# Kernel optimization log

Measured on AMD Instinct MI355X. Metric: run time of the kernel, lower is better.

## Reference

```python
import jax, jax.numpy as jnp
import numpy as np

S, N, LAT, HID, NH, NLAYERS = 8, 128, 128, 384, 8, 6
HT, WT, DT = 128, 128, 128
DIN, DOUT, RAD, LEVELS, FED = 1169, 3 + 3 * 128, 3, 4, 64


def sincos1d(d, pos):
    # MAE-style 1d sincos embedding, d even -> [..., d]
    omega = 1.0 / (10000.0 ** (jnp.arange(d // 2, dtype=jnp.float32) / (d / 2.0)))
    ang = pos[..., None] * omega
    return jnp.concatenate([jnp.sin(ang), jnp.cos(ang)], axis=-1)


def flow_embed(f, Cd=FED):
    # get_3d_embedding(flows, 64, cat_coords=True) -> [..., 3*Cd+3] = 195
    div = jnp.arange(0, Cd, 2, dtype=jnp.float32) * (1000.0 / Cd)
    outs = []
    for a in range(3):
        ang = f[..., a, None] * div
        pe = jnp.stack([jnp.sin(ang), jnp.cos(ang)], axis=-1).reshape(f.shape[:-1] + (Cd,))
        outs.append(pe)
    return jnp.concatenate(outs + [f], axis=-1)


def avg_pool2(x):
    B, Sv, Cc, H, W = x.shape
    return x.reshape(B, Sv, Cc, H // 2, 2, W // 2, 2).mean(axis=(4, 6))


def pyramid(fm):
    pyr = [fm]
    for _ in range(LEVELS - 1):
        fm = avg_pool2(fm)
        pyr.append(fm)
    return pyr


def bilinear_sample(corr, xy):
    # corr: [B,S,N,H,W]; xy: [B,S,N,P,2] pixel coords (x indexes W, y indexes H); zero padding
    B, Sv, Nn, H, W = corr.shape
    cf = corr.reshape(B, Sv, Nn, H * W)
    x, y = xy[..., 0], xy[..., 1]
    x0f = jnp.floor(x); y0f = jnp.floor(y)
    wx, wy = x - x0f, y - y0f
    x0 = x0f.astype(jnp.int32); y0 = y0f.astype(jnp.int32)

    def gather(xi, yi):
        ok = ((xi >= 0) & (xi < W) & (yi >= 0) & (yi < H)).astype(cf.dtype)
        idx = jnp.clip(yi, 0, H - 1) * W + jnp.clip(xi, 0, W - 1)
        v = jnp.take_along_axis(cf, idx.reshape(B, Sv, Nn, -1), axis=-1).reshape(idx.shape)
        return v * ok

    v00 = gather(x0, y0); v01 = gather(x0 + 1, y0)
    v10 = gather(x0, y0 + 1); v11 = gather(x0 + 1, y0 + 1)
    return v00 * (1 - wx) * (1 - wy) + v01 * wx * (1 - wy) + v10 * (1 - wx) * wy + v11 * wx * wy


def corr_sample(pyr, targets, coords):
    # RAFT/CoTracker CorrBlock: per-level dense correlation then (2r+1)^2 window bilinear lookup
    d = jnp.arange(-RAD, RAD + 1, dtype=jnp.float32)
    delta = jnp.stack(jnp.meshgrid(d, d, indexing="ij"), axis=-1).reshape(-1, 2)  # [49,2]
    scale = 1.0 / jnp.sqrt(jnp.float32(targets.shape[-1]))
    outs = []
    for l, fm in enumerate(pyr):
        corr = jnp.einsum("bsnc,bschw->bsnhw", targets, fm) * scale
        xy = coords[..., None, :] / (2.0 ** l) + delta
        outs.append(bilinear_sample(corr, xy))
    return jnp.concatenate(outs, axis=-1)  # [B,S,N,196]


def layernorm(x, g, b):
    m = x.mean(-1, keepdims=True)
    v = x.var(-1, keepdims=True)
    return (x - m) / jnp.sqrt(v + 1e-5) * g + b


def attention(x, Wqkv, bq, Wo, bo):
    M, T, H = x.shape
    dh = H // NH
    qkv = (x @ Wqkv + bq).reshape(M, T, 3, NH, dh)
    q, k, v = qkv[:, :, 0], qkv[:, :, 1], qkv[:, :, 2]
    att = jax.nn.softmax(jnp.einsum("mthd,mshd->mhts", q, k) / jnp.sqrt(jnp.float32(dh)), axis=-1)
    o = jnp.einsum("mhts,mshd->mthd", att, v).reshape(M, T, H)
    return o @ Wo + bo


def updateformer(x, support, W_in, b_in, lnp, Wqkv, bqkv, Wo, bo, W1, b1, W2, b2, W_out, b_out, Ws, bs):
    # x: [B,N,T,DIN]; alternating time (over T) and space (over N) pre-LN transformer blocks
    B, Np, T, _ = x.shape
    sproj = support @ Ws + bs  # [100,HID]
    h = x @ W_in + b_in + sproj.mean(axis=0)
    for i in range(NLAYERS):
        g1, bb1, g2, bb2 = lnp[i, 0], lnp[i, 1], lnp[i, 2], lnp[i, 3]
        if i % 2 == 0:
            y = h.reshape(B * Np, T, HID)
        else:
            y = h.transpose(0, 2, 1, 3).reshape(B * T, Np, HID)
        y = y + attention(layernorm(y, g1, bb1), Wqkv[i], bqkv[i], Wo[i], bo[i])
        z = layernorm(y, g2, bb2)
        y = y + jax.nn.gelu(z @ W1[i] + b1[i], approximate=False) @ W2[i] + b2[i]
        if i % 2 == 0:
            h = y.reshape(B, Np, T, HID)
        else:
            h = y.reshape(B, T, Np, HID).transpose(0, 2, 1, 3)
    return h @ W_out + b_out, sproj[None]


def groupnorm1(x, g, b):
    m = x.mean(-1, keepdims=True)
    v = x.var(-1, keepdims=True)
    return (x - m) / jnp.sqrt(v + 1e-5) * g + b


def _forward(fmapXY, fmapYZ, fmapXZ, coords_init, vis_init, track_mask, feat_init, support_features,
             W_in, b_in, lnp, Wqkv, bqkv, Wo, bo, W1, b1, W2, b2, W_out, b_out, Ws, bs,
             gn_g, gn_b, Wu, bu, Wvis, bvis, iters):
    B, Sv, Cc, H, W = fmapXY.shape
    D = fmapXZ.shape[-2]
    Nn = coords_init.shape[2]
    coords = coords_init
    ffeats = [feat_init[..., k] for k in range(3)]
    pyrXY, pyrYZ, pyrXZ = pyramid(fmapXY), pyramid(fmapYZ), pyramid(fmapXZ)
    grid_size = jnp.array([H, W, D], dtype=jnp.float32)
    # 3d sincos pos embed from query coords; 1169 padded to 1170 -> 390/axis, truncated back
    g = (coords[:, 0] / grid_size * 2.0 - 1.0) * 128.0  # [B,N,3]
    pe = jnp.concatenate([sincos1d(390, g[..., i]) for i in range(3)], axis=-1)[..., :DIN]
    pos_embed = pe.reshape(B * Nn, 1, DIN)
    times_embed = sincos1d(1170, jnp.arange(Sv, dtype=jnp.float32))[None, :, :DIN]
    support = support_features
    for _ in range(iters):
        coords = jax.lax.stop_gradient(coords)  # matches coords.detach()
        fxy = corr_sample(pyrXY, ffeats[0], coords[..., :2])
        fyz = corr_sample(pyrYZ, ffeats[1], coords[..., 1:3])
        fxz = corr_sample(pyrXZ, ffeats[2], coords[..., 0::2])
        fcorrs = jnp.concatenate([fxy, fyz, fxz], axis=-1)  # [B,S,N,588]
        fcorrs_ = fcorrs.transpose(0, 2, 1, 3).reshape(B * Nn, Sv, -1)
        flows_ = (coords - coords[:, :1]).transpose(0, 2, 1, 3).reshape(B * Nn, Sv, 3)
        flows_cat = flow_embed(flows_)  # [BN,S,195]
        ff = [f.transpose(0, 2, 1, 3).reshape(B * Nn, Sv, LAT) for f in ffeats]
        ffeats_ = jnp.concatenate(ff, axis=-1)  # [BN,S,384]
        # replicate torch's cat(dim=2)+permute+reshape layout exactly
        tmv = jnp.concatenate([track_mask, vis_init], axis=2).transpose(0, 2, 1, 3).reshape(B * Nn, Sv, 2)
        tin = jnp.concatenate([flows_cat, fcorrs_, ffeats_, tmv], axis=-1)  # [BN,S,1169]
        x = (tin + pos_embed + times_embed).reshape(B, Nn, Sv, DIN)
        delta, dse3 = updateformer(x, support, W_in, b_in, lnp, Wqkv, bqkv, Wo, bo, W1, b1, W2, b2, W_out, b_out, Ws, bs)
        support = support + dse3[0] / 100.0
        delta = delta.reshape(B * Nn, Sv, DOUT)
        d_coord = delta[..., :3].reshape(B, Nn, Sv, 3).transpose(0, 2, 1, 3)
        coords = coords + d_coord
        new_ffeats = []
        for k in range(3):
            dfk = delta[..., 3 + k * LAT:3 + (k + 1) * LAT]
            upd = jax.nn.gelu(groupnorm1(dfk, gn_g[k], gn_b[k]) @ Wu[k] + bu[k], approximate=False)
            new_ffeats.append(ffeats[k] + upd.reshape(B, Nn, Sv, LAT).transpose(0, 2, 1, 3))
        ffeats = new_ffeats
    vis = (jnp.concatenate(ffeats, axis=-1) @ Wvis + bvis)[..., 0]  # [B,S,N]
    return jnp.concatenate([coords, vis[..., None]], axis=-1)  # [B,S,N,4]


def setup_inputs() -> dict:
    key = jax.random.key(0)
    ks = jax.random.split(key, 16)
    f32 = jnp.float32
    B = 1
    fmapXY = jax.random.normal(ks[0], (B, S, LAT, HT, WT), f32)
    fmapYZ = jax.random.normal(ks[1], (B, S, LAT, DT, HT), f32)
    fmapXZ = jax.random.normal(ks[2], (B, S, LAT, DT, WT), f32)
    coords_init = jax.random.uniform(ks[3], (B, S, N, 3), f32) * 112.0 + 8.0
    vis_init = jnp.ones((B, S, N, 1), f32)
    track_mask = jnp.ones((B, S, N, 1), f32)
    feat_init = jax.random.normal(ks[4], (B, S, N, LAT, 3), f32)
    support_features = jnp.zeros((100, HID), f32) + 0.1
    w = lambda k, sh: jax.random.normal(k, sh, f32) * 0.02
    ln1 = jnp.stack([jnp.ones(HID, f32), jnp.zeros(HID, f32), jnp.ones(HID, f32), jnp.zeros(HID, f32)])
    params = dict(
        W_in=w(ks[5], (DIN, HID)), b_in=jnp.zeros((HID,), f32),
        lnp=jnp.tile(ln1[None], (NLAYERS, 1, 1)),
        Wqkv=w(ks[6], (NLAYERS, HID, 3 * HID)), bqkv=jnp.zeros((NLAYERS, 3 * HID), f32),
        Wo=w(ks[7], (NLAYERS, HID, HID)), bo=jnp.zeros((NLAYERS, HID), f32),
        W1=w(ks[8], (NLAYERS, HID, 4 * HID)), b1=jnp.zeros((NLAYERS, 4 * HID), f32),
        W2=w(ks[9], (NLAYERS, 4 * HID, HID)), b2=jnp.zeros((NLAYERS, HID), f32),
        W_out=w(ks[10], (HID, DOUT)), b_out=jnp.zeros((DOUT,), f32),
        Ws=w(ks[11], (HID, HID)), bs=jnp.zeros((HID,), f32),
        gn_g=jnp.ones((3, LAT), f32), gn_b=jnp.zeros((3, LAT), f32),
        Wu=w(ks[12], (3, LAT, LAT)), bu=jnp.zeros((3, LAT), f32),
        Wvis=w(ks[13], (3 * LAT, 1)), bvis=jnp.zeros((1,), f32),
    )
    return dict(fmapXY=fmapXY, fmapYZ=fmapYZ, fmapXZ=fmapXZ, coords_init=coords_init,
                vis_init=vis_init, track_mask=track_mask, feat_init=feat_init,
                support_features=support_features, iters=2, **params)


def reference(fmapXY, fmapYZ, fmapXZ, coords_init, vis_init, track_mask, feat_init, support_features,
              W_in, b_in, lnp, Wqkv, bqkv, Wo, bo, W1, b1, W2, b2, W_out, b_out, Ws, bs,
              gn_g, gn_b, Wu, bu, Wvis, bvis, iters):
    return _forward(fmapXY, fmapYZ, fmapXZ, coords_init, vis_init, track_mask, feat_init, support_features,
                    W_in, b_in, lnp, Wqkv, bqkv, Wo, bo, W1, b1, W2, b2, W_out, b_out, Ws, bs,
                    gn_g, gn_b, Wu, bu, Wvis, bvis, iters)
```

## Files before the change

### kernel.cpp

```cpp
#include <hip/hip_runtime.h>
#include <hip/hip_bf16.h>


#define DEVFN __device__ __forceinline__

typedef __attribute__((ext_vector_type(8))) short short8;
typedef __attribute__((ext_vector_type(4))) float f32x4;

static constexpr float INV_SQRT_DH = 0.14433756729740643f;
static constexpr float CORR_SCALE  = 0.08838834764831845f;
static constexpr size_t VSTRIDE = 22282240;

DEVFN float gelu_exact(float x){
  return 0.5f * x * (1.0f + erff(x * 0.7071067811865476f));
}
DEVFN short bf16_of(float f){
  __hip_bfloat16 b = __float2bfloat16(f);
  return *reinterpret_cast<short*>(&b);
}
DEVFN float bfu(uint32_t u16){ return __uint_as_float(u16 << 16); }


__global__ void init_state_k(float* coords, const float* cinit,
                             float* ff, const float* feat_init,
                             float* support, const float* sfeat){
  int idx = blockIdx.x*256 + threadIdx.x;
  if (idx < 3072)  coords[idx]  = cinit[idx];
  if (idx < 49152){
    int row = idx / 384;
    support[idx] = (row < 100) ? sfeat[idx] : 0.0f;
  }
  if (idx < 393216){
    int k = idx / 131072, rest = idx % 131072;
    ff[idx] = feat_init[(size_t)rest*3 + k];
  }
}

__global__ void build_posE_k(float* posE, const float* cinit){
  int idx = blockIdx.x*256 + threadIdx.x;
  if (idx >= 128*1169) return;
  int n = idx / 1169, d = idx % 1169;
  int i = d / 390, dd = d % 390;
  float c = cinit[n*3 + i];
  float g = (c / 128.0f * 2.0f - 1.0f) * 128.0f;
  int m = (dd < 195) ? dd : dd - 195;
  float om = powf(10000.0f, -(float)m / 195.0f);
  float ang = g * om;
  posE[idx] = (dd < 195) ? sinf(ang) : cosf(ang);
}

__global__ void build_timE_k(float* timE){
  int idx = blockIdx.x*256 + threadIdx.x;
  if (idx >= 8*1169) return;
  int s = idx / 1169, d = idx % 1169;
  int m = (d < 585) ? d : d - 585;
  float om = powf(10000.0f, -(float)m / 585.0f);
  float ang = (float)s * om;
  timE[idx] = (d < 585) ? sinf(ang) : cosf(ang);
}

__global__ void transpose_cl_k(const float* __restrict__ in, __hip_bfloat16* __restrict__ out){
  __shared__ float tile[32][33];
  int s = blockIdx.z;
  int c0 = blockIdx.y*32, h0 = blockIdx.x*32;
  int tx = threadIdx.x & 31, ty = threadIdx.x >> 5;
  const float* ib = in + (size_t)s*128*16384;
  #pragma unroll
  for (int r=0;r<4;r++){
    int c = c0 + ty + r*8;
    tile[ty + r*8][tx] = ib[(size_t)c*16384 + h0 + tx];
  }
  __syncthreads();
  __hip_bfloat16* ob = out + (size_t)s*16384*128;
  #pragma unroll
  for (int r=0;r<4;r++){
    int hw = h0 + ty + r*8;
    ob[(size_t)hw*128 + c0 + tx] = __float2bfloat16(tile[tx][ty + r*8]);
  }
}

__global__ void pool2_k(const __hip_bfloat16* __restrict__ in, __hip_bfloat16* __restrict__ out, int So){
  int idx = blockIdx.x*256 + threadIdx.x;
  int total = 8*So*So*128;
  if (idx >= total) return;
  int c = idx & 127;
  int x = (idx >> 7) % So;
  int y = ((idx >> 7) / So) % So;
  int s = idx / (So*So*128);
  int Si = So*2;
  const __hip_bfloat16* b0 = in + (((size_t)s*Si + 2*y)*Si + 2*x)*128 + c;
  float v = __bfloat162float(b0[0]) + __bfloat162float(b0[128])
          + __bfloat162float(b0[(size_t)Si*128]) + __bfloat162float(b0[(size_t)Si*128 + 128]);
  out[idx] = __float2bfloat16(v*0.25f);
}

__global__ void wtrans_k(const float* __restrict__ in, __hip_bfloat16* __restrict__ out,
                         int K, int N, int Kpad, int Npad){
  __shared__ float tile[32][33];
  int z = blockIdx.z;
  const float* ib = in + (size_t)z*K*N;
  __hip_bfloat16* ob = out + (size_t)z*Npad*Kpad;
  int kb = blockIdx.y*32, nb = blockIdx.x*32;
  int tx = threadIdx.x & 31, ty = threadIdx.x >> 5;
  #pragma unroll
  for (int r=0;r<4;r++){
    int k = kb + ty + r*8, n = nb + tx;
    tile[ty+r*8][tx] = (k < K && n < N) ? ib[(size_t)k*N + n] : 0.0f;
  }
  __syncthreads();
  #pragma unroll
  for (int r=0;r<4;r++){
    int n = nb + ty + r*8, k = kb + tx;
    if (n < Npad && k < Kpad) ob[(size_t)n*Kpad + k] = __float2bfloat16(tile[tx][ty+r*8]);
  }
}

__global__ void assemble_x_k(__hip_bfloat16* __restrict__ xbuf, const float* __restrict__ posE,
                             const float* __restrict__ timE, const float* __restrict__ coords,
                             const float* __restrict__ ff, const float* __restrict__ tmask,
                             const float* __restrict__ vinit){
  int r = blockIdx.x;
  int n = r >> 3, s = r & 7;
  for (int d = threadIdx.x; d < 1184; d += blockDim.x){
    __hip_bfloat16* dst = xbuf + (size_t)r*1184 + d;
    if (d >= 1169){ *dst = __float2bfloat16(0.0f); continue; }
    float base = posE[(size_t)n*1169 + d] + timE[(size_t)s*1169 + d];
    if (d >= 195 && d < 783){ *dst = __float2bfloat16(base); continue; }
    float val;
    if (d < 195){
      if (d >= 192){
        int a = d - 192;
        val = coords[(s*128+n)*3 + a] - coords[n*3 + a];
      } else {
        int a = d >> 6, dd = d & 63;
        float f = coords[(s*128+n)*3 + a] - coords[n*3 + a];
        float ang = f * (31.25f * (float)(dd >> 1));
        val = (dd & 1) ? cosf(ang) : sinf(ang);
      }
    } else if (d < 1167){
      int cidx = d - 783, k = cidx >> 7, cc = cidx & 127;
      val = ff[(size_t)k*131072 + (size_t)(s*128+n)*128 + cc];
    } else {
      int c = d - 1167;
      int flat = n*16 + s*2 + c;
      int n2 = flat >> 3, s2 = flat & 7;
      val = (n2 < 128) ? tmask[s2*128 + n2] : vinit[s2*128 + (n2-128)];
    }
    *dst = __float2bfloat16(val + base);
  }
}

__global__ void corr_k(const __hip_bfloat16* __restrict__ pyr, const float* __restrict__ coords,
                       const float* __restrict__ ff, __hip_bfloat16* __restrict__ xbuf){
  __shared__ float t[128];
  __shared__ float p[64];
  int bid = blockIdx.x;
  int view = bid >> 10, s = (bid >> 7) & 7, n = bid & 127;
  int tid = threadIdx.x;
  t[tid]      = ff[(size_t)view*131072 + (size_t)(s*128+n)*128 + tid];
  t[tid + 64] = ff[(size_t)view*131072 + (size_t)(s*128+n)*128 + tid + 64];
  int ax = (view==1) ? 1 : 0;
  int ay = (view==0) ? 1 : 2;
  float X = coords[(s*128+n)*3 + ax];
  float Y = coords[(s*128+n)*3 + ay];
  const __hip_bfloat16* vb = pyr + (size_t)view*VSTRIDE;
  __syncthreads();
  size_t loff = 0;
  for (int l=0;l<4;l++){
    int sz = 128 >> l;
    float inv = 1.0f / (float)(1 << l);
    float cx = X * inv, cy = Y * inv;
    float x0f = floorf(cx), y0f = floorf(cy);
    float wx = cx - x0f, wy = cy - y0f;
    int ix0 = (int)x0f, iy0 = (int)y0f;
    int px = ix0 - 3 + (tid & 7);
    int py = iy0 - 3 + (tid >> 3);
    float acc = 0.0f;
    if (px >= 0 && px < sz && py >= 0 && py < sz){
      const uint2* row = reinterpret_cast<const uint2*>(vb + loff + (((size_t)s*sz + py)*sz + px)*128);
      #pragma unroll
      for (int c4=0;c4<32;c4++){
        uint2 u = row[c4];
        float f0 = __uint_as_float(u.x << 16);
        float f1 = __uint_as_float(u.x & 0xffff0000u);
        float f2 = __uint_as_float(u.y << 16);
        float f3 = __uint_as_float(u.y & 0xffff0000u);
        acc += t[c4*4+0]*f0 + t[c4*4+1]*f1 + t[c4*4+2]*f2 + t[c4*4+3]*f3;
      }
    }
    p[tid] = acc;
    __syncthreads();
    if (tid < 49){
      int i = tid / 7, jj = tid % 7;
      float v = p[jj*8+i]       * (1.0f-wx)*(1.0f-wy)
              + p[jj*8+i+1]     * wx*(1.0f-wy)
              + p[(jj+1)*8+i]   * (1.0f-wx)*wy
              + p[(jj+1)*8+i+1] * wx*wy;
      __hip_bfloat16* dst = xbuf + (size_t)(n*8+s)*1184 + 195 + view*196 + l*49 + tid;
      *dst = __float2bfloat16(__bfloat162float(*dst) + v * CORR_SCALE);
    }
    loff += (size_t)8*sz*sz*128;
    __syncthreads();
  }
}

__global__ void gn_rows_k(const float* __restrict__ dbuf,
                          const float* __restrict__ gn_g, const float* __restrict__ gn_b,
                          __hip_bfloat16* __restrict__ gtmp, float* __restrict__ coords){
  int k = blockIdx.y;
  const float* in = dbuf + 3 + k*128;
  const float* g = gn_g + k*128;
  const float* b = gn_b + k*128;
  __hip_bfloat16* out = gtmp + (size_t)k*131072;
  int wave = threadIdx.x >> 6, lane = threadIdx.x & 63;
  int r = blockIdx.x*4 + wave;
  const float* row = in + (size_t)r*387;
  float x0 = row[lane], x1 = row[lane+64];
  float sum = x0 + x1;
  #pragma unroll
  for (int o=32;o>0;o>>=1) sum += __shfl_xor(sum, o);
  float mean = sum / 128.0f;
  float d0 = x0-mean, d1 = x1-mean;
  float vs = d0*d0 + d1*d1;
  #pragma unroll
  for (int o=32;o>0;o>>=1) vs += __shfl_xor(vs, o);
  float invstd = 1.0f / sqrtf(vs/128.0f + 1e-5f);
  out[(size_t)r*128 + lane]      = __float2bfloat16(d0*invstd*g[lane] + b[lane]);
  out[(size_t)r*128 + lane + 64] = __float2bfloat16(d1*invstd*g[lane+64] + b[lane+64]);
  if (k == 0 && blockIdx.x < 12){
    int idx = blockIdx.x*256 + threadIdx.x;
    if (idx < 3072){
      int a = idx % 3, sn = idx / 3;
      int ss = sn >> 7, nn = sn & 127;
      coords[idx] += dbuf[(size_t)(nn*8+ss)*387 + a];
    }
  }
}

template<int K, int MODE, bool AF32>
__global__ __launch_bounds__(256) void mgemm_k(const void* __restrict__ A, int lda,
                                               const __hip_bfloat16* __restrict__ Bt,
                                               float* __restrict__ C, int ldc,
                                               int M, int N,
                                               const float* __restrict__ bias){
  constexpr int NSTEP = K/32;
  int tid = threadIdx.x;
  int lane = tid & 63, wid = tid >> 6;
  int wr = wid >> 1, wc = wid & 1;
  int lr = lane & 15, lk = lane >> 4;
  int m0 = blockIdx.y*64 + wr*32;
  int n0 = blockIdx.x*64 + wc*32;

  const __hip_bfloat16* Ab = (const __hip_bfloat16*)A;
  const float* Af = (const float*)A;
  size_t arow0 = (size_t)(m0 + lr)      * lda;
  size_t arow1 = (size_t)(m0 + 16 + lr) * lda;
  size_t brow0 = (size_t)(n0 + lr)      * K;
  size_t brow1 = (size_t)(n0 + 16 + lr) * K;

  f32x4 acc00 = {}, acc01 = {}, acc10 = {}, acc11 = {};

  auto loadAf = [&](size_t rowoff, int k0)->short8{
    if constexpr (AF32){
      const float* p = Af + rowoff + k0 + lk*8;
      short8 r;
      #pragma unroll
      for (int j=0;j<8;j++) r[j] = bf16_of(p[j]);
      return r;
    } else {
      return *reinterpret_cast<const short8*>(Ab + rowoff + k0 + lk*8);
    }
  };
  auto loadBf = [&](size_t rowoff, int k0)->short8{
    return *reinterpret_cast<const short8*>(Bt + rowoff + k0 + lk*8);
  };

  short8 a0 = loadAf(arow0,0), a1 = loadAf(arow1,0);
  short8 b0 = loadBf(brow0,0), b1 = loadBf(brow1,0);
  #pragma unroll
  for (int t=0;t<NSTEP;t++){
    short8 na0={}, na1={}, nb0={}, nb1={};
    if (t+1 < NSTEP){
      int k0 = (t+1)*32;
      na0 = loadAf(arow0,k0); na1 = loadAf(arow1,k0);
      nb0 = loadBf(brow0,k0); nb1 = loadBf(brow1,k0);
    }
    acc00 = __builtin_amdgcn_mfma_f32_16x16x32_bf16(a0,b0,acc00,0,0,0);
    acc01 = __builtin_amdgcn_mfma_f32_16x16x32_bf16(a0,b1,acc01,0,0,0);
    acc10 = __builtin_amdgcn_mfma_f32_16x16x32_bf16(a1,b0,acc10,0,0,0);
    acc11 = __builtin_amdgcn_mfma_f32_16x16x32_bf16(a1,b1,acc11,0,0,0);
    a0=na0; a1=na1; b0=nb0; b1=nb1;
  }

  f32x4 accs[2][2] = {{acc00, acc01},{acc10, acc11}};
  #pragma unroll
  for (int mi=0;mi<2;mi++){
    #pragma unroll
    for (int ni=0;ni<2;ni++){
      int c = n0 + ni*16 + lr;
      if (c >= N) continue;
      float bv = bias ? bias[c] : 0.0f;
      #pragma unroll
      for (int reg=0;reg<4;reg++){
        int r = m0 + mi*16 + lk*4 + reg;
        if (r >= M) continue;
        float v = accs[mi][ni][reg] + bv;
        if (MODE==0) C[(size_t)r*ldc + c] = v;
        else C[(size_t)r*ldc + c] += v;
      }
    }
  }
}

template<bool GELU>
__global__ __launch_bounds__(256) void lngemm_k(const float* __restrict__ A,
                                                const float* __restrict__ gamma,
                                                const float* __restrict__ beta,
                                                const __hip_bfloat16* __restrict__ Bt,
                                                __hip_bfloat16* __restrict__ Cbf, int ldc, int N,
                                                const float* __restrict__ bias){
  constexpr int LDSS = 392;
  __shared__ short Asm[64*LDSS];
  int tid = threadIdx.x, lane = tid & 63, w = tid >> 6;
  int m0 = blockIdx.y*64, n0b = blockIdx.x*64;

  float gg[6], bb[6];
  #pragma unroll
  for (int e=0;e<6;e++){ gg[e] = gamma[lane+e*64]; bb[e] = beta[lane+e*64]; }
  for (int rr=0; rr<16; rr++){
    int r = w*16 + rr;
    const float* row = A + (size_t)(m0+r)*384;
    float x[6]; float sum = 0.0f;
    #pragma unroll
    for (int e=0;e<6;e++){ x[e] = row[lane+e*64]; sum += x[e]; }
    #pragma unroll
    for (int o=32;o>0;o>>=1) sum += __shfl_xor(sum, o);
    float mean = sum * (1.0f/384.0f);
    float vs = 0.0f;
    #pragma unroll
    for (int e=0;e<6;e++){ float d = x[e]-mean; vs += d*d; }
    #pragma unroll
    for (int o=32;o>0;o>>=1) vs += __shfl_xor(vs, o);
    float invstd = 1.0f / sqrtf(vs*(1.0f/384.0f) + 1e-5f);
    #pragma unroll
    for (int e=0;e<6;e++)
      Asm[r*LDSS + lane + e*64] = bf16_of((x[e]-mean)*invstd*gg[e] + bb[e]);
  }
  __syncthreads();

  int wr = w >> 1, wc = w & 1;
  int lr = lane & 15, lk = lane >> 4;
  const __hip_bfloat16* Brow0 = Bt + (size_t)(n0b + wc*32 + lr)*384;
  const __hip_bfloat16* Brow1 = Brow0 + 16*384;
  short8 b0 = *(const short8*)(Brow0 + lk*8);
  short8 b1 = *(const short8*)(Brow1 + lk*8);
  f32x4 acc00={}, acc01={}, acc10={}, acc11={};
  #pragma unroll
  for (int t=0;t<12;t++){
    short8 a0 = *(const short8*)(&Asm[(wr*32+lr)*LDSS    + t*32 + lk*8]);
    short8 a1 = *(const short8*)(&Asm[(wr*32+16+lr)*LDSS + t*32 + lk*8]);
    short8 nb0={}, nb1={};
    if (t < 11){
      nb0 = *(const short8*)(Brow0 + (t+1)*32 + lk*8);
      nb1 = *(const short8*)(Brow1 + (t+1)*32 + lk*8);
    }
    acc00 = __builtin_amdgcn_mfma_f32_16x16x32_bf16(a0,b0,acc00,0,0,0);
    acc01 = __builtin_amdgcn_mfma_f32_16x16x32_bf16(a0,b1,acc01,0,0,0);
    acc10 = __builtin_amdgcn_mfma_f32_16x16x32_bf16(a1,b0,acc10,0,0,0);
    acc11 = __builtin_amdgcn_mfma_f32_16x16x32_bf16(a1,b1,acc11,0,0,0);
    b0=nb0; b1=nb1;
  }
  f32x4 accs[2][2] = {{acc00, acc01},{acc10, acc11}};
  #pragma unroll
  for (int mi=0;mi<2;mi++){
    #pragma unroll
    for (int ni=0;ni<2;ni++){
      int c = n0b + wc*32 + ni*16 + lr;
      float bv = bias[c];
      #pragma unroll
      for (int reg=0;reg<4;reg++){
        int r = m0 + wr*32 + mi*16 + lk*4 + reg;
        float v = accs[mi][ni][reg] + bv;
        Cbf[(size_t)r*ldc + c] = __float2bfloat16(GELU ? gelu_exact(v) : v);
      }
    }
  }
}

__global__ __launch_bounds__(256) void wu_gemm_k(const __hip_bfloat16* __restrict__ gtmp,
                                                 const __hip_bfloat16* __restrict__ WuT,
                                                 const float* __restrict__ bu,
                                                 float* __restrict__ ff){
  int z = blockIdx.z;
  const __hip_bfloat16* A  = gtmp + (size_t)z*131072;
  const __hip_bfloat16* Bt = WuT  + (size_t)z*16384;
  const float* bias = bu + (size_t)z*128;
  float* aux = ff + (size_t)z*131072;
  int tid = threadIdx.x, lane = tid & 63, wid = tid >> 6;
  int wr = wid >> 1, wc = wid & 1;
  int lr = lane & 15, lk = lane >> 4;
  int m0 = blockIdx.y*64 + wr*32;
  int n0 = blockIdx.x*64 + wc*32;
  const short8* A0 = (const short8*)(A + (size_t)(m0+lr)*128);
  const short8* A1 = (const short8*)(A + (size_t)(m0+16+lr)*128);
  const short8* B0 = (const short8*)(Bt + (size_t)(n0+lr)*128);
  const short8* B1 = (const short8*)(Bt + (size_t)(n0+16+lr)*128);
  f32x4 acc00={}, acc01={}, acc10={}, acc11={};
  #pragma unroll
  for (int t=0;t<4;t++){
    short8 a0 = A0[t*4 + lk], a1 = A1[t*4 + lk];
    short8 b0 = B0[t*4 + lk], b1 = B1[t*4 + lk];
    acc00 = __builtin_amdgcn_mfma_f32_16x16x32_bf16(a0,b0,acc00,0,0,0);
    acc01 = __builtin_amdgcn_mfma_f32_16x16x32_bf16(a0,b1,acc01,0,0,0);
    acc10 = __builtin_amdgcn_mfma_f32_16x16x32_bf16(a1,b0,acc10,0,0,0);
    acc11 = __builtin_amdgcn_mfma_f32_16x16x32_bf16(a1,b1,acc11,0,0,0);
  }
  f32x4 accs[2][2] = {{acc00, acc01},{acc10, acc11}};
  #pragma unroll
  for (int mi=0;mi<2;mi++){
    #pragma unroll
    for (int ni=0;ni<2;ni++){
      int c = n0 + ni*16 + lr;
      float bv = bias[c];
      #pragma unroll
      for (int reg=0;reg<4;reg++){
        int r = m0 + mi*16 + lk*4 + reg;
        float v = accs[mi][ni][reg] + bv;
        int ss = r & 7, nn2 = r >> 3;
        aux[((size_t)(ss*128+nn2))*128 + c] += gelu_exact(v);
      }
    }
  }
}

__global__ __launch_bounds__(512) void attn_even_k(const __hip_bfloat16* __restrict__ qkv,
                                                   __hip_bfloat16* __restrict__ attout){
  int g = blockIdx.x;
  int h = threadIdx.x >> 6;
  int lane = threadIdx.x & 63;
  int t = lane >> 3, j = lane & 7;
  const short* qs = (const short*)qkv;

  float q[48], kk[48];
  {
    const short8* qp = (const short8*)(qs + (size_t)(g*8+t)*1152 + h*48);
    const short8* kp = (const short8*)(qs + (size_t)(g*8+j)*1152 + 384 + h*48);
    #pragma unroll
    for (int c=0;c<6;c++){
      short8 qv = qp[c], kv = kp[c];
      #pragma unroll
      for (int e=0;e<8;e++){
        q[c*8+e]  = bfu((uint16_t)qv[e]);
        kk[c*8+e] = bfu((uint16_t)kv[e]);
      }
    }
  }
  float s = 0.0f;
  #pragma unroll
  for (int d=0;d<48;d++) s += q[d]*kk[d];
  s *= INV_SQRT_DH;
  float mx = s;
  #pragma unroll
  for (int o=1;o<8;o<<=1) mx = fmaxf(mx, __shfl_xor(mx, o));
  float e = expf(s - mx);
  float l = e;
  #pragma unroll
  for (int o=1;o<8;o<<=1) l += __shfl_xor(l, o);
  float p = e / l;

  float o6[6] = {0,0,0,0,0,0};
  #pragma unroll
  for (int jp=0;jp<8;jp++){
    float pj = __shfl(p, (lane & 56) | jp);
    const uint32_t* vp = (const uint32_t*)(qs + (size_t)(g*8+jp)*1152 + 768 + h*48 + j*6);
    uint32_t w0 = vp[0], w1 = vp[1], w2 = vp[2];
    o6[0] += pj * bfu(w0 & 0xffffu); o6[1] += pj * bfu(w0 >> 16);
    o6[2] += pj * bfu(w1 & 0xffffu); o6[3] += pj * bfu(w1 >> 16);
    o6[4] += pj * bfu(w2 & 0xffffu); o6[5] += pj * bfu(w2 >> 16);
  }
  uint32_t r0 = ((uint32_t)(uint16_t)bf16_of(o6[1]) << 16) | (uint16_t)bf16_of(o6[0]);
  uint32_t r1 = ((uint32_t)(uint16_t)bf16_of(o6[3]) << 16) | (uint16_t)bf16_of(o6[2]);
  uint32_t r2 = ((uint32_t)(uint16_t)bf16_of(o6[5]) << 16) | (uint16_t)bf16_of(o6[4]);
  uint32_t* op = (uint32_t*)((short*)attout + (size_t)(g*8+t)*384 + h*48 + j*6);
  op[0] = r0; op[1] = r1; op[2] = r2;
}

__global__ __launch_bounds__(256) void attn_odd_mfma_k(const __hip_bfloat16* __restrict__ qkv,
                                                       __hip_bfloat16* __restrict__ attout){
  __shared__ char smem[47872];
  short* Qb = (short*)smem;
  short* Kb = (short*)(smem + 18432);
  short* Pb = (short*)smem;
  short* Vt = (short*)(smem + 34816);
  int g = blockIdx.x & 7, h = blockIdx.x >> 3;
  int tid = threadIdx.x;

  const short* qs = (const short*)qkv;
  for (int idx = tid; idx < 768; idx += 256){
    int t = idx / 6, dblk = idx % 6;
    size_t base = (size_t)(t*8+g)*1152 + h*48 + dblk*8;
    *(short8*)(Qb + t*72 + dblk*8) = *(const short8*)(qs + base);
    *(short8*)(Kb + t*72 + dblk*8) = *(const short8*)(qs + base + 384);
  }
  short8 zz = {};
  for (int idx = tid; idx < 384; idx += 256){
    int t = idx / 3, dblk = idx % 3;
    *(short8*)(Qb + t*72 + 48 + dblk*8) = zz;
    *(short8*)(Kb + t*72 + 48 + dblk*8) = zz;
  }
  __syncthreads();

  int lane = tid & 63, w = tid >> 6;
  int lr = lane & 15, lk = lane >> 4;
  int m0 = w*32;

  f32x4 S[2][8] = {};
  #pragma unroll
  for (int ks=0; ks<2; ks++){
    short8 a0 = *(const short8*)(Qb + (m0+lr)*72    + ks*32 + lk*8);
    short8 a1 = *(const short8*)(Qb + (m0+16+lr)*72 + ks*32 + lk*8);
    #pragma unroll
    for (int ni=0; ni<8; ni++){
      short8 b = *(const short8*)(Kb + (ni*16+lr)*72 + ks*32 + lk*8);
      S[0][ni] = __builtin_amdgcn_mfma_f32_16x16x32_bf16(a0,b,S[0][ni],0,0,0);
      S[1][ni] = __builtin_amdgcn_mfma_f32_16x16x32_bf16(a1,b,S[1][ni],0,0,0);
    }
  }

  #pragma unroll
  for (int mi=0;mi<2;mi++){
    #pragma unroll
    for (int reg=0;reg<4;reg++){
      float m = -1e30f;
      #pragma unroll
      for (int ni=0;ni<8;ni++) m = fmaxf(m, S[mi][ni][reg]);
      #pragma unroll
      for (int o=1;o<16;o<<=1) m = fmaxf(m, __shfl_xor(m, o));
      m *= INV_SQRT_DH;
      float l = 0.0f;
      #pragma unroll
      for (int ni=0;ni<8;ni++){
        float p = expf(S[mi][ni][reg]*INV_SQRT_DH - m);
        S[mi][ni][reg] = p;
        l += p;
      }
      #pragma unroll
      for (int o=1;o<16;o<<=1) l += __shfl_xor(l, o);
      float inv = 1.0f/l;
      #pragma unroll
      for (int ni=0;ni<8;ni++) S[mi][ni][reg] *= inv;
    }
  }
  __syncthreads();

  for (int idx = tid; idx < 768; idx += 256){
    int j = idx / 6, dblk = idx % 6;
    short8 v = *(const short8*)(qs + (size_t)(j*8+g)*1152 + 768 + h*48 + dblk*8);
    #pragma unroll
    for (int e=0;e<8;e++) Vt[(dblk*8+e)*136 + j] = v[e];
  }
  #pragma unroll
  for (int mi=0;mi<2;mi++)
    #pragma unroll
    for (int ni=0;ni<8;ni++)
      #pragma unroll
      for (int reg=0;reg<4;reg++)
        Pb[(m0+mi*16+lk*4+reg)*136 + ni*16+lr] = bf16_of(S[mi][ni][reg]);
  __syncthreads();

  f32x4 O[2][3] = {};
  #pragma unroll
  for (int ks=0; ks<4; ks++){
    short8 a0 = *(const short8*)(Pb + (m0+lr)*136    + ks*32 + lk*8);
    short8 a1 = *(const short8*)(Pb + (m0+16+lr)*136 + ks*32 + lk*8);
    #pragma unroll
    for (int ni=0; ni<3; ni++){
      short8 b = *(const short8*)(Vt + (ni*16+lr)*136 + ks*32 + lk*8);
      O[0][ni] = __builtin_amdgcn_mfma_f32_16x16x32_bf16(a0,b,O[0][ni],0,0,0);
      O[1][ni] = __builtin_amdgcn_mfma_f32_16x16x32_bf16(a1,b,O[1][ni],0,0,0);
    }
  }
  #pragma unroll
  for (int mi=0;mi<2;mi++){
    #pragma unroll
    for (int ni=0;ni<3;ni++){
      #pragma unroll
      for (int reg=0;reg<4;reg++){
        int q = m0 + mi*16 + lk*4 + reg;
        int d = ni*16 + lr;
        attout[(size_t)(q*8+g)*384 + h*48 + d] = __float2bfloat16(O[mi][ni][reg]);
      }
    }
  }
}

__global__ void supp_smean_k(const float* __restrict__ sproj, const float* __restrict__ b_in,
                             float* __restrict__ bias2, float* __restrict__ support){
  int idx = blockIdx.x*256 + threadIdx.x;
  if (idx < 38400) support[idx] += sproj[idx]*0.01f;
  else if (idx < 38784){
    int c = idx - 38400;
    float s = 0.0f;
    for (int r=0;r<100;r++) s += sproj[r*384 + c];
    bias2[c] = b_in[c] + s*0.01f;
  }
}

__global__ void final_out_k(const float* __restrict__ coords, const float* __restrict__ ff,
                            const float* __restrict__ Wvis, const float* __restrict__ bvis,
                            float* __restrict__ out){
  int sn = blockIdx.x*64 + threadIdx.x;
  if (sn >= 1024) return;
  float acc = bvis[0];
  for (int k=0;k<3;k++)
    for (int c=0;c<128;c++)
      acc += ff[(size_t)k*131072 + (size_t)sn*128 + c] * Wvis[k*128 + c];
  out[sn*4+0] = coords[sn*3+0];
  out[sn*4+1] = coords[sn*3+1];
  out[sn*4+2] = coords[sn*3+2];
  out[sn*4+3] = acc;
}


extern "C" void kernel_launch(void* const* d_in, const int* in_sizes, int n_in,
                              void* d_out, int out_size, void* d_ws, size_t ws_size,
                              hipStream_t stream) {
  const float* fmapXY   = (const float*)d_in[0];
  const float* fmapYZ   = (const float*)d_in[1];
  const float* fmapXZ   = (const float*)d_in[2];
  const float* cinit    = (const float*)d_in[3];
  const float* vinit    = (const float*)d_in[4];
  const float* tmask    = (const float*)d_in[5];
  const float* feat_init= (const float*)d_in[6];
  const float* sfeat    = (const float*)d_in[7];
  const float* W_in     = (const float*)d_in[9];
  const float* b_in     = (const float*)d_in[10];
  const float* lnp      = (const float*)d_in[11];
  const float* Wqkv     = (const float*)d_in[12];
  const float* bqkv     = (const float*)d_in[13];
  const float* Wo       = (const float*)d_in[14];
  const float* bo       = (const float*)d_in[15];
  const float* W1       = (const float*)d_in[16];
  const float* b1       = (const float*)d_in[17];
  const float* W2       = (const float*)d_in[18];
  const float* b2       = (const float*)d_in[19];
  const float* W_out    = (const float*)d_in[20];
  const float* b_out    = (const float*)d_in[21];
  const float* Ws       = (const float*)d_in[22];
  const float* bs       = (const float*)d_in[23];
  const float* gn_g     = (const float*)d_in[24];
  const float* gn_b     = (const float*)d_in[25];
  const float* Wu       = (const float*)d_in[26];
  const float* bu       = (const float*)d_in[27];
  const float* Wvis     = (const float*)d_in[28];
  const float* bvis     = (const float*)d_in[29];
  const int ITERS = 2;

  char* wp = (char*)d_ws;
  auto alloc = [&](size_t bytes)->char* {
    char* p = wp; wp += (bytes + 255) & ~(size_t)255; return p;
  };
  __hip_bfloat16* pyr = (__hip_bfloat16*)alloc(3ull*VSTRIDE*2);
  float* coords = (float*)alloc(3072ull*4);
  float* ff     = (float*)alloc(393216ull*4);
  float* support= (float*)alloc(49152ull*4);
  float* sproj  = (float*)alloc(38400ull*4);
  float* bias2  = (float*)alloc(384ull*4);
  float* posE   = (float*)alloc(149632ull*4);
  float* timE   = (float*)alloc(9352ull*4);
  float* h      = (float*)alloc(393216ull*4);
  float* dbuf   = (float*)alloc(396288ull*4);
  __hip_bfloat16* xbuf_bf = (__hip_bfloat16*)alloc(1212416ull*2);
  __hip_bfloat16* qkv_bf  = (__hip_bfloat16*)alloc(1179648ull*2);
  __hip_bfloat16* atto_bf = (__hip_bfloat16*)alloc(393216ull*2);
  __hip_bfloat16* ffb_bf  = (__hip_bfloat16*)alloc(1572864ull*2);
  __hip_bfloat16* gtmp_bf = (__hip_bfloat16*)alloc(393216ull*2);
  __hip_bfloat16* WsT   = (__hip_bfloat16*)alloc(147456ull*2);
  __hip_bfloat16* WinT  = (__hip_bfloat16*)alloc(454656ull*2);
  __hip_bfloat16* WqkvT = (__hip_bfloat16*)alloc(2654208ull*2);
  __hip_bfloat16* WoT   = (__hip_bfloat16*)alloc(884736ull*2);
  __hip_bfloat16* W1T   = (__hip_bfloat16*)alloc(3538944ull*2);
  __hip_bfloat16* W2T   = (__hip_bfloat16*)alloc(3538944ull*2);
  __hip_bfloat16* WoutT = (__hip_bfloat16*)alloc(172032ull*2);
  __hip_bfloat16* WuT   = (__hip_bfloat16*)alloc(49152ull*2);
  if ((size_t)(wp - (char*)d_ws) > ws_size) return;

  init_state_k<<<1536, 256, 0, stream>>>(coords, cinit, ff, feat_init, support, sfeat);
  build_posE_k<<<(128*1169 + 255)/256, 256, 0, stream>>>(posE, cinit);
  build_timE_k<<<(8*1169 + 255)/256, 256, 0, stream>>>(timE);

  const float* fmaps[3] = {fmapXY, fmapYZ, fmapXZ};
  for (int v=0; v<3; v++){
    __hip_bfloat16* base = pyr + (size_t)v*VSTRIDE;
    transpose_cl_k<<<dim3(512,4,8), 256, 0, stream>>>(fmaps[v], base);
    pool2_k<<<(8*64*64*128 + 255)/256, 256, 0, stream>>>(base,              base + 16777216, 64);
    pool2_k<<<(8*32*32*128 + 255)/256, 256, 0, stream>>>(base + 16777216,   base + 20971520, 32);
    pool2_k<<<(8*16*16*128 + 255)/256, 256, 0, stream>>>(base + 20971520,   base + 22020096, 16);
  }

  wtrans_k<<<dim3(12,12,1), 256, 0, stream>>>(Ws,    WsT,   384, 384, 384, 384);
  wtrans_k<<<dim3(12,37,1), 256, 0, stream>>>(W_in,  WinT,  1169,384, 1184,384);
  wtrans_k<<<dim3(36,12,6), 256, 0, stream>>>(Wqkv,  WqkvT, 384, 1152,384, 1152);
  wtrans_k<<<dim3(12,12,6), 256, 0, stream>>>(Wo,    WoT,   384, 384, 384, 384);
  wtrans_k<<<dim3(48,12,6), 256, 0, stream>>>(W1,    W1T,   384, 1536,384, 1536);
  wtrans_k<<<dim3(12,48,6), 256, 0, stream>>>(W2,    W2T,   1536,384, 1536,384);
  wtrans_k<<<dim3(14,12,1), 256, 0, stream>>>(W_out, WoutT, 384, 387, 384, 448);
  wtrans_k<<<dim3(4,4,3),   256, 0, stream>>>(Wu,    WuT,   128, 128, 128, 128);

  for (int it=0; it<ITERS; ++it){
    assemble_x_k<<<1024, 256, 0, stream>>>(xbuf_bf, posE, timE, coords, ff, tmask, vinit);
    corr_k<<<3072, 64, 0, stream>>>(pyr, coords, ff, xbuf_bf);

    mgemm_k<384,0,true><<<dim3(6,2), 256, 0, stream>>>(support,384, WsT, sproj,384, 100,384, bs);
    supp_smean_k<<<152, 256, 0, stream>>>(sproj, b_in, bias2, support);

    mgemm_k<1184,0,false><<<dim3(6,16), 256, 0, stream>>>(xbuf_bf,1184, WinT, h,384, 1024,384, bias2);

    for (int i=0;i<6;i++){
      const float* g1  = lnp + (size_t)(i*4+0)*384;
      const float* bb1 = lnp + (size_t)(i*4+1)*384;
      const float* g2  = lnp + (size_t)(i*4+2)*384;
      const float* bb2 = lnp + (size_t)(i*4+3)*384;

      lngemm_k<false><<<dim3(18,16), 256, 0, stream>>>(h, g1, bb1, WqkvT + (size_t)i*442368,
                                                       qkv_bf, 1152, 1152, bqkv + i*1152);
      if ((i & 1) == 0) attn_even_k<<<128, 512, 0, stream>>>(qkv_bf, atto_bf);
      else              attn_odd_mfma_k<<<64, 256, 0, stream>>>(qkv_bf, atto_bf);
      mgemm_k<384,1,false><<<dim3(6,16), 256, 0, stream>>>(atto_bf,384, WoT + (size_t)i*147456,
                                                           h,384, 1024,384, bo + i*384);
      lngemm_k<true><<<dim3(24,16), 256, 0, stream>>>(h, g2, bb2, W1T + (size_t)i*589824,
                                                      ffb_bf, 1536, 1536, b1 + i*1536);
      mgemm_k<1536,1,false><<<dim3(6,16), 256, 0, stream>>>(ffb_bf,1536, W2T + (size_t)i*589824,
                                                            h,384, 1024,384, b2 + i*384);
    }

    mgemm_k<384,0,true><<<dim3(7,16), 256, 0, stream>>>(h,384, WoutT, dbuf,387, 1024,387, b_out);
    gn_rows_k<<<dim3(256,3), 256, 0, stream>>>(dbuf, gn_g, gn_b, gtmp_bf, coords);
    wu_gemm_k<<<dim3(2,16,3), 256, 0, stream>>>(gtmp_bf, WuT, bu, ff);
  }

  final_out_k<<<16, 64, 0, stream>>>(coords, ff, Wvis, bvis, (float*)d_out);
}
```

Before: 1.451 ms.

## Batch pyramid build across views, deepen GEMM prefetch, widen LN-GEMM tiles

Merges the per-view transpose and pooling launches into single launches that index the view through blockIdx.z, cutting launch count. The mgemm kernel now prefetches three K-steps ahead instead of one, to hide global load latency. lngemm widens each block to 128 output columns, each wave computing 4 N fragments with double-buffered B loads. The block count halves, so the LayerNorm prologue runs half as often, but fewer blocks run at once and register pressure rises.

```diff
diff --git a/kernel.cpp b/kernel.cpp
--- a/kernel.cpp
+++ b/kernel.cpp
@@ -59,9 +59,11 @@
   timE[idx] = (d < 585) ? sinf(ang) : cosf(ang);
 }
 
-__global__ void transpose_cl_k(const float* __restrict__ in, __hip_bfloat16* __restrict__ out){
+__global__ void transpose_cl_k(const float* __restrict__ inXY, const float* __restrict__ inYZ,
+                               const float* __restrict__ inXZ, __hip_bfloat16* __restrict__ pyr){
   __shared__ float tile[32][33];
-  int s = blockIdx.z;
+  int v = blockIdx.z >> 3, s = blockIdx.z & 7;
+  const float* in = (v==0) ? inXY : ((v==1) ? inYZ : inXZ);
   int c0 = blockIdx.y*32, h0 = blockIdx.x*32;
   int tx = threadIdx.x & 31, ty = threadIdx.x >> 5;
   const float* ib = in + (size_t)s*128*16384;
@@ -71,7 +73,7 @@
     tile[ty + r*8][tx] = ib[(size_t)c*16384 + h0 + tx];
   }
   __syncthreads();
-  __hip_bfloat16* ob = out + (size_t)s*16384*128;
+  __hip_bfloat16* ob = pyr + (size_t)v*VSTRIDE + (size_t)s*16384*128;
   #pragma unroll
   for (int r=0;r<4;r++){
     int hw = h0 + ty + r*8;
@@ -79,10 +81,12 @@
   }
 }
 
-__global__ void pool2_k(const __hip_bfloat16* __restrict__ in, __hip_bfloat16* __restrict__ out, int So){
+__global__ void pool2_k(__hip_bfloat16* __restrict__ pyr, size_t in_off, size_t out_off, int So){
   int idx = blockIdx.x*256 + threadIdx.x;
   int total = 8*So*So*128;
   if (idx >= total) return;
+  const __hip_bfloat16* in = pyr + (size_t)blockIdx.z*VSTRIDE + in_off;
+  __hip_bfloat16* out      = pyr + (size_t)blockIdx.z*VSTRIDE + out_off;
   int c = idx & 127;
   int x = (idx >> 7) % So;
   int y = ((idx >> 7) / So) % So;
@@ -258,38 +262,42 @@
   size_t brow0 = (size_t)(n0 + lr)      * K;
   size_t brow1 = (size_t)(n0 + 16 + lr) * K;
 
-  f32x4 acc00 = {}, acc01 = {}, acc10 = {}, acc11 = {};
-
-  auto loadAf = [&](size_t rowoff, int k0)->short8{
+  auto loadA = [&](size_t ro, int k0)->short8{
     if constexpr (AF32){
-      const float* p = Af + rowoff + k0 + lk*8;
+      const float* p = Af + ro + k0 + lk*8;
       short8 r;
       #pragma unroll
       for (int j=0;j<8;j++) r[j] = bf16_of(p[j]);
       return r;
     } else {
-      return *reinterpret_cast<const short8*>(Ab + rowoff + k0 + lk*8);
+      return *reinterpret_cast<const short8*>(Ab + ro + k0 + lk*8);
     }
   };
-  auto loadBf = [&](size_t rowoff, int k0)->short8{
-    return *reinterpret_cast<const short8*>(Bt + rowoff + k0 + lk*8);
+  auto loadB = [&](size_t ro, int k0)->short8{
+    return *reinterpret_cast<const short8*>(Bt + ro + k0 + lk*8);
   };
 
-  short8 a0 = loadAf(arow0,0), a1 = loadAf(arow1,0);
-  short8 b0 = loadBf(brow0,0), b1 = loadBf(brow1,0);
+  short8 a0[3], a1[3], b0[3], b1[3];
+  #pragma unroll
+  for (int p=0;p<3;p++){
+    if (p < NSTEP){
+      a0[p]=loadA(arow0,p*32); a1[p]=loadA(arow1,p*32);
+      b0[p]=loadB(brow0,p*32); b1[p]=loadB(brow1,p*32);
+    }
+  }
+  f32x4 acc00 = {}, acc01 = {}, acc10 = {}, acc11 = {};
   #pragma unroll
   for (int t=0;t<NSTEP;t++){
-    short8 na0={}, na1={}, nb0={}, nb1={};
-    if (t+1 < NSTEP){
-      int k0 = (t+1)*32;
-      na0 = loadAf(arow0,k0); na1 = loadAf(arow1,k0);
-      nb0 = loadBf(brow0,k0); nb1 = loadBf(brow1,k0);
-    }
-    acc00 = __builtin_amdgcn_mfma_f32_16x16x32_bf16(a0,b0,acc00,0,0,0);
-    acc01 = __builtin_amdgcn_mfma_f32_16x16x32_bf16(a0,b1,acc01,0,0,0);
-    acc10 = __builtin_amdgcn_mfma_f32_16x16x32_bf16(a1,b0,acc10,0,0,0);
-    acc11 = __builtin_amdgcn_mfma_f32_16x16x32_bf16(a1,b1,acc11,0,0,0);
-    a0=na0; a1=na1; b0=nb0; b1=nb1;
+    const int cur = t % 3;
+    acc00 = __builtin_amdgcn_mfma_f32_16x16x32_bf16(a0[cur],b0[cur],acc00,0,0,0);
+    acc01 = __builtin_amdgcn_mfma_f32_16x16x32_bf16(a0[cur],b1[cur],acc01,0,0,0);
+    acc10 = __builtin_amdgcn_mfma_f32_16x16x32_bf16(a1[cur],b0[cur],acc10,0,0,0);
+    acc11 = __builtin_amdgcn_mfma_f32_16x16x32_bf16(a1[cur],b1[cur],acc11,0,0,0);
+    if (t+3 < NSTEP){
+      int k0 = (t+3)*32;
+      a0[cur]=loadA(arow0,k0); a1[cur]=loadA(arow1,k0);
+      b0[cur]=loadB(brow0,k0); b1[cur]=loadB(brow1,k0);
+    }
   }
 
   f32x4 accs[2][2] = {{acc00, acc01},{acc10, acc11}};
@@ -317,12 +325,12 @@
                                                 const float* __restrict__ gamma,
                                                 const float* __restrict__ beta,
                                                 const __hip_bfloat16* __restrict__ Bt,
-                                                __hip_bfloat16* __restrict__ Cbf, int ldc, int N,
+                                                __hip_bfloat16* __restrict__ Cbf, int ldc,
                                                 const float* __restrict__ bias){
   constexpr int LDSS = 392;
   __shared__ short Asm[64*LDSS];
   int tid = threadIdx.x, lane = tid & 63, w = tid >> 6;
-  int m0 = blockIdx.y*64, n0b = blockIdx.x*64;
+  int m0 = blockIdx.y*64, n0b = blockIdx.x*128;
 
   float gg[6], bb[6];
   #pragma unroll
@@ -350,37 +358,44 @@
 
   int wr = w >> 1, wc = w & 1;
   int lr = lane & 15, lk = lane >> 4;
-  const __hip_bfloat16* Brow0 = Bt + (size_t)(n0b + wc*32 + lr)*384;
-  const __hip_bfloat16* Brow1 = Brow0 + 16*384;
-  short8 b0 = *(const short8*)(Brow0 + lk*8);
-  short8 b1 = *(const short8*)(Brow1 + lk*8);
-  f32x4 acc00={}, acc01={}, acc10={}, acc11={};
+  const __hip_bfloat16* Brow[4];
+  #pragma unroll
+  for (int ni=0;ni<4;ni++) Brow[ni] = Bt + (size_t)(n0b + wc*64 + ni*16 + lr)*384;
+
+  short8 bfrag[2][4];
+  #pragma unroll
+  for (int p=0;p<2;p++)
+    #pragma unroll
+    for (int ni=0;ni<4;ni++)
+      bfrag[p][ni] = *(const short8*)(Brow[ni] + p*32 + lk*8);
+
+  f32x4 acc[2][4] = {};
   #pragma unroll
   for (int t=0;t<12;t++){
+    const int cur = t & 1;
     short8 a0 = *(const short8*)(&Asm[(wr*32+lr)*LDSS    + t*32 + lk*8]);
     short8 a1 = *(const short8*)(&Asm[(wr*32+16+lr)*LDSS + t*32 + lk*8]);
-    short8 nb0={}, nb1={};
-    if (t < 11){
-      nb0 = *(const short8*)(Brow0 + (t+1)*32 + lk*8);
-      nb1 = *(const short8*)(Brow1 + (t+1)*32 + lk*8);
-    }
-    acc00 = __builtin_amdgcn_mfma_f32_16x16x32_bf16(a0,b0,acc00,0,0,0);
-    acc01 = __builtin_amdgcn_mfma_f32_16x16x32_bf16(a0,b1,acc01,0,0,0);
-    acc10 = __builtin_amdgcn_mfma_f32_16x16x32_bf16(a1,b0,acc10,0,0,0);
-    acc11 = __builtin_amdgcn_mfma_f32_16x16x32_bf16(a1,b1,acc11,0,0,0);
-    b0=nb0; b1=nb1;
-  }
-  f32x4 accs[2][2] = {{acc00, acc01},{acc10, acc11}};
+    #pragma unroll
+    for (int ni=0;ni<4;ni++){
+      acc[0][ni] = __builtin_amdgcn_mfma_f32_16x16x32_bf16(a0,bfrag[cur][ni],acc[0][ni],0,0,0);
+      acc[1][ni] = __builtin_amdgcn_mfma_f32_16x16x32_bf16(a1,bfrag[cur][ni],acc[1][ni],0,0,0);
+    }
+    if (t+2 < 12){
+      #pragma unroll
+      for (int ni=0;ni<4;ni++)
+        bfrag[cur][ni] = *(const short8*)(Brow[ni] + (t+2)*32 + lk*8);
+    }
+  }
   #pragma unroll
   for (int mi=0;mi<2;mi++){
     #pragma unroll
-    for (int ni=0;ni<2;ni++){
-      int c = n0b + wc*32 + ni*16 + lr;
+    for (int ni=0;ni<4;ni++){
+      int c = n0b + wc*64 + ni*16 + lr;
       float bv = bias[c];
       #pragma unroll
       for (int reg=0;reg<4;reg++){
         int r = m0 + wr*32 + mi*16 + lk*4 + reg;
-        float v = accs[mi][ni][reg] + bv;
+        float v = acc[mi][ni][reg] + bv;
         Cbf[(size_t)r*ldc + c] = __float2bfloat16(GELU ? gelu_exact(v) : v);
       }
     }
@@ -689,14 +704,10 @@
   build_posE_k<<<(128*1169 + 255)/256, 256, 0, stream>>>(posE, cinit);
   build_timE_k<<<(8*1169 + 255)/256, 256, 0, stream>>>(timE);
 
-  const float* fmaps[3] = {fmapXY, fmapYZ, fmapXZ};
-  for (int v=0; v<3; v++){
-    __hip_bfloat16* base = pyr + (size_t)v*VSTRIDE;
-    transpose_cl_k<<<dim3(512,4,8), 256, 0, stream>>>(fmaps[v], base);
-    pool2_k<<<(8*64*64*128 + 255)/256, 256, 0, stream>>>(base,              base + 16777216, 64);
-    pool2_k<<<(8*32*32*128 + 255)/256, 256, 0, stream>>>(base + 16777216,   base + 20971520, 32);
-    pool2_k<<<(8*16*16*128 + 255)/256, 256, 0, stream>>>(base + 20971520,   base + 22020096, 16);
-  }
+  transpose_cl_k<<<dim3(512,4,24), 256, 0, stream>>>(fmapXY, fmapYZ, fmapXZ, pyr);
+  pool2_k<<<dim3((8*64*64*128 + 255)/256,1,3), 256, 0, stream>>>(pyr, 0,        16777216, 64);
+  pool2_k<<<dim3((8*32*32*128 + 255)/256,1,3), 256, 0, stream>>>(pyr, 16777216, 20971520, 32);
+  pool2_k<<<dim3((8*16*16*128 + 255)/256,1,3), 256, 0, stream>>>(pyr, 20971520, 22020096, 16);
 
   wtrans_k<<<dim3(12,12,1), 256, 0, stream>>>(Ws,    WsT,   384, 384, 384, 384);
   wtrans_k<<<dim3(12,37,1), 256, 0, stream>>>(W_in,  WinT,  1169,384, 1184,384);
@@ -722,14 +733,14 @@
       const float* g2  = lnp + (size_t)(i*4+2)*384;
       const float* bb2 = lnp + (size_t)(i*4+3)*384;
 
-      lngemm_k<false><<<dim3(18,16), 256, 0, stream>>>(h, g1, bb1, WqkvT + (size_t)i*442368,
-                                                       qkv_bf, 1152, 1152, bqkv + i*1152);
+      lngemm_k<false><<<dim3(9,16), 256, 0, stream>>>(h, g1, bb1, WqkvT + (size_t)i*442368,
+                                                      qkv_bf, 1152, bqkv + i*1152);
       if ((i & 1) == 0) attn_even_k<<<128, 512, 0, stream>>>(qkv_bf, atto_bf);
       else              attn_odd_mfma_k<<<64, 256, 0, stream>>>(qkv_bf, atto_bf);
       mgemm_k<384,1,false><<<dim3(6,16), 256, 0, stream>>>(atto_bf,384, WoT + (size_t)i*147456,
                                                            h,384, 1024,384, bo + i*384);
-      lngemm_k<true><<<dim3(24,16), 256, 0, stream>>>(h, g2, bb2, W1T + (size_t)i*589824,
-                                                      ffb_bf, 1536, 1536, b1 + i*1536);
+      lngemm_k<true><<<dim3(12,16), 256, 0, stream>>>(h, g2, bb2, W1T + (size_t)i*589824,
+                                                      ffb_bf, 1536, b1 + i*1536);
       mgemm_k<1536,1,false><<<dim3(6,16), 256, 0, stream>>>(ffb_bf,1536, W2T + (size_t)i*589824,
                                                             h,384, 1024,384, b2 + i*384);
     }
```

Measured after the change: 1.459 ms. No clear change (+0.6%).
